# Kernel tuning notes

Measured on AMD Instinct MI355X. Metric: run time of the kernel, lower is better.

## Reference

```python
import jax, jax.numpy as jnp
import numpy as np

N = 4096
C = 64
B = 4
DIST_THRESHOLD = 0.5
ALPHA = 0.01
NEG_INF = -1e15


def setup_inputs() -> dict:
    key = jax.random.key(0)
    k1, k2, k3, k4, k5 = jax.random.split(key, 5)
    x = jax.random.normal(k1, (B, N, C), dtype=jnp.float32)
    dist_mat = jax.random.uniform(k2, (N, N), dtype=jnp.float32)
    proj_w = jax.random.normal(k3, (N, C, C), dtype=jnp.float32) / np.sqrt(C)
    proj_b = jax.random.normal(k4, (N, C), dtype=jnp.float32) * 0.01
    a_w = jax.random.normal(k5, (N, 2 * C), dtype=jnp.float32) / np.sqrt(2 * C)
    return {"x": x, "dist_mat": dist_mat, "proj_w": proj_w, "proj_b": proj_b, "a_w": a_w}


def reference(x, dist_mat, proj_w, proj_b, a_w):
    # Adjacency: (0 < dist < threshold), diagonal forced to 1.
    adj = (dist_mat > 0) & (dist_mat < DIST_THRESHOLD)
    adj = adj | jnp.eye(N, dtype=bool)

    # Per-node projection (GraphDense): h[b,n,:] = x[b,n,:] @ proj_w[n] + proj_b[n]
    h = jnp.einsum('bnc,nco->bno', x, proj_w) + proj_b  # [B, N, C]

    # Attention score: a[j] . concat(h_i, h_j) without materializing [B,N,N,2C].
    a_src, a_dst = a_w[:, :C], a_w[:, C:]               # each [N, C]
    s = jnp.einsum('bic,jc->bij', h, a_src) + jnp.einsum('bjc,jc->bj', h, a_dst)[:, None, :]
    s = jnp.where(s >= 0, s, ALPHA * s)                 # LeakyReLU
    s = jnp.where(adj[None, :, :], s, NEG_INF)          # mask non-edges
    att = jax.nn.softmax(s, axis=-1)                    # [B, N, N]

    # Weighted aggregation over neighbors.
    y = jnp.einsum('bij,bjc->bic', att, h)              # [B, N, C]
    return y
```

## Files before the change

### kernel.cpp

```cpp
#include <hip/hip_runtime.h>

#define N 4096
#define C 64
#define B 4
#define SHIFT 12.0f

typedef __attribute__((ext_vector_type(8))) short short8;
typedef __attribute__((ext_vector_type(4))) short s16x4;
typedef __attribute__((ext_vector_type(4))) float f32x4;
typedef unsigned long long u64;

#define MFMA16(a, b, c) __builtin_amdgcn_mfma_f32_16x16x32_bf16(a, b, c, 0, 0, 0)

__device__ __forceinline__ short f2bf(float f) {
    unsigned u = __builtin_bit_cast(unsigned, f);
    u += 0x7fffu + ((u >> 16) & 1u);
    return (short)(u >> 16);
}

__global__ __launch_bounds__(256) void mask_kernel(const float* __restrict__ dist,
                                                   u64* __restrict__ msk) {
    const int wave = threadIdx.x >> 6, lane = threadIdx.x & 63;
    const int i = blockIdx.x * 4 + wave;
    const float* row = dist + (size_t)i * N;
#pragma unroll 8
    for (int jb = 0; jb < N / 64; jb++) {
        float d = row[jb * 64 + lane];
        u64 m = __ballot(d > 0.f && d < 0.5f);
        int dj = i - jb * 64;
        if (dj >= 0 && dj < 64) m |= (1ull << dj);
        if (lane == 0) msk[(size_t)i * (N / 64) + jb] = m;
    }
}

__global__ __launch_bounds__(256) void proj_kernel(
    const float* __restrict__ x,
    const float* __restrict__ proj_w,
    const float* __restrict__ proj_b,
    const float* __restrict__ a_w,
    short* __restrict__ h_bf,
    short* __restrict__ a_srcb,
    float* __restrict__ e2)
{
    __shared__ float lds_w[4][64 * 64];
    __shared__ float lds_x[4][B][C];

    const int tid = threadIdx.x;
    const int wave = tid >> 6;
    const int lane = tid & 63;
    const int n = blockIdx.x * 4 + wave;
    const float* Wn = proj_w + (size_t)n * C * C;

    float4 wbuf[16];
#pragma unroll
    for (int it = 0; it < 16; it++)
        wbuf[it] = *(const float4*)(Wn + it * 256 + lane * 4);
#pragma unroll
    for (int b = 0; b < B; b++)
        lds_x[wave][b][lane] = x[((size_t)b * N + n) * C + lane];
#pragma unroll
    for (int it = 0; it < 16; it++)
        *(float4*)&lds_w[wave][it * 256 + lane * 4] = wbuf[it];

    const int o = lane;
    float acc[B];
    float pb = proj_b[(size_t)n * C + o];
#pragma unroll
    for (int b = 0; b < B; b++) acc[b] = pb;

#pragma unroll 4
    for (int c4 = 0; c4 < C; c4 += 4) {
        f32x4 xq[B];
#pragma unroll
        for (int b = 0; b < B; b++) xq[b] = *(const f32x4*)&lds_x[wave][b][c4];
#pragma unroll
        for (int k = 0; k < 4; k++) {
            float w = lds_w[wave][(c4 + k) * C + o];
#pragma unroll
            for (int b = 0; b < B; b++) acc[b] = fmaf(xq[b][k], w, acc[b]);
        }
    }

    float adst = a_w[(size_t)n * (2 * C) + C + o];
    a_srcb[(size_t)n * C + o] = f2bf(a_w[(size_t)n * (2 * C) + o]);
#pragma unroll
    for (int b = 0; b < B; b++) {
        h_bf[((size_t)b * N + n) * C + o] = f2bf(acc[b]);
        float prod = acc[b] * adst;
#pragma unroll
        for (int off = 32; off; off >>= 1) prod += __shfl_xor(prod, off, 64);
        if (lane == 0) e2[b * N + n] = prod - SHIFT;
    }
}

__global__ __launch_bounds__(256) void transpose_kernel(const short* __restrict__ h_bf,
                                                        short* __restrict__ hT_bf) {
    __shared__ short tile[64][72];
    const int t = threadIdx.x;
    const int b = blockIdx.y;
    const int n0 = blockIdx.x * 64;
    {
        int r = t >> 2, cs = (t & 3) * 16;
        const short* src = h_bf + ((size_t)b * N + n0 + r) * C + cs;
#pragma unroll
        for (int q = 0; q < 4; q++)
            *(s16x4*)&tile[r][cs + q * 4] = *(const s16x4*)(src + q * 4);
    }
    __syncthreads();
    {
        int c = t >> 2, ns = (t & 3) * 16;
        short v[16];
#pragma unroll
        for (int k = 0; k < 16; k++) v[k] = tile[ns + k][c];
        short* dst = hT_bf + (size_t)b * C * N + (size_t)c * N + n0 + ns;
        *(short8*)dst = *(short8*)&v[0];
        *(short8*)(dst + 8) = *(short8*)&v[8];
    }
}

__global__ __launch_bounds__(256) void attn_kernel(
    const u64* __restrict__ msk,
    const short* __restrict__ h_bf,
    const short* __restrict__ hT_bf,
    const short* __restrict__ a_srcb,
    const float* __restrict__ e2,
    float* __restrict__ part_y,
    float* __restrict__ part_l,
    int JS, int S, int mode)
{
    __shared__ float lds_e2[4][512];

    const int tid = threadIdx.x;
    const int wave = tid >> 6;
    const int lane = tid & 63;
    const int cl = lane & 15;
    const int rg = lane >> 4;
    const int rg8 = rg * 8;
    const int b = wave;
    const int sy = blockIdx.x % S;
    const int ix = blockIdx.x / S;
    const int i0 = ix * 32;
    const int jbeg = sy * JS;
    const bool e2lds = (JS <= 512);

    if (e2lds) {
        for (int q = lane * 4; q < JS; q += 256)
            *(f32x4*)&lds_e2[wave][q] = *(const f32x4*)(e2 + (size_t)b * N + jbeg + q);
    }

    short8 bfr[2][2];
#pragma unroll
    for (int u = 0; u < 2; u++) {
        const short* hrow = h_bf + ((size_t)b * N + i0 + u * 16 + cl) * C;
        bfr[u][0] = *(const short8*)(hrow + rg8);
        bfr[u][1] = *(const short8*)(hrow + 32 + rg8);
    }

    const u64* mr[2] = {msk + (size_t)(i0 + cl) * (N / 64),
                        msk + (size_t)(i0 + 16 + cl) * (N / 64)};

    f32x4 yacc[2][4];
#pragma unroll
    for (int u = 0; u < 2; u++)
#pragma unroll
        for (int t = 0; t < 4; t++) { f32x4 z = {0.f, 0.f, 0.f, 0.f}; yacc[u][t] = z; }
    float l_s[2] = {0.f, 0.f};

    const int jr = ((cl >> 2) << 3) | (cl & 3);
    const short* abase = a_srcb + (size_t)(jr) * C + rg8;

    short8 an0[4], an1[4];
#pragma unroll
    for (int t = 0; t < 4; t++) {
        const short* arow = abase + (size_t)(jbeg + (t >> 1) * 32 + (t & 1) * 4) * C;
        an0[t] = *(const short8*)(arow);
        an1[t] = *(const short8*)(arow + 32);
    }
    u64 mb0 = mr[0][jbeg >> 6], mb1 = mr[1][jbeg >> 6];

    for (int j0 = jbeg; j0 < jbeg + JS; j0 += 64) {
        const int jp = (j0 + 64 < jbeg + JS) ? j0 + 64 : jbeg;
        const u64 mb[2] = {mb0, mb1};

        short8 a0[4], a1[4];
#pragma unroll
        for (int t = 0; t < 4; t++) { a0[t] = an0[t]; a1[t] = an1[t]; }

        short8 h0[4], h1[4];
#pragma unroll
        for (int t = 0; t < 4; t++) {
            const short* hc = hT_bf + (size_t)b * C * N + (size_t)(t * 16 + cl) * N + j0 + rg8;
            h0[t] = *(const short8*)(hc);
            h1[t] = *(const short8*)(hc + 32);
        }
#pragma unroll
        for (int t = 0; t < 4; t++) {
            const short* arow = abase + (size_t)(jp + (t >> 1) * 32 + (t & 1) * 4) * C;
            an0[t] = *(const short8*)(arow);
            an1[t] = *(const short8*)(arow + 32);
        }
        u64 nb0 = mr[0][jp >> 6], nb1 = mr[1][jp >> 6];

        f32x4 st[2][4];
#pragma unroll
        for (int t = 0; t < 4; t++) {
            const int tq = t >> 1, tr = t & 1;
            const int off = tq * 32 + tr * 4 + rg8;
            f32x4 eq;
            if (e2lds) eq = *(const f32x4*)&lds_e2[wave][j0 - jbeg + off];
            else       eq = *(const f32x4*)(e2 + (size_t)b * N + j0 + off);
            const int sh = rg8 + tr * 4;
#pragma unroll
            for (int u = 0; u < 2; u++) {
                unsigned w32 = tq ? (unsigned)(mb[u] >> 32) : (unsigned)mb[u];
                unsigned ws = w32 >> sh;
                f32x4 z;
#pragma unroll
                for (int r = 0; r < 4; r++)
                    z[r] = ((ws >> r) & 1u) ? eq[r] : -1e30f;
                z = MFMA16(a0[t], bfr[u][0], z);
                z = MFMA16(a1[t], bfr[u][1], z);
                st[u][t] = z;
            }
        }

        short8 pa[2][2];
#pragma unroll
        for (int u = 0; u < 2; u++) {
            float ls = 0.f;
            short8 q0, q1;
#pragma unroll
            for (int t = 0; t < 4; t++) {
#pragma unroll
                for (int r = 0; r < 4; r++) {
                    float sv = st[u][t][r];
                    float pv = __expf(fmaxf(sv, fmaf(0.01f, sv, -11.88f)));
                    ls += pv;
                    short bv = f2bf(pv);
                    if (t < 2) q0[(t & 1) * 4 + r] = bv;
                    else       q1[(t & 1) * 4 + r] = bv;
                }
            }
            l_s[u] += ls;
            pa[u][0] = q0;
            pa[u][1] = q1;
        }

#pragma unroll
        for (int t = 0; t < 4; t++) {
            yacc[0][t] = MFMA16(pa[0][0], h0[t], yacc[0][t]);
            yacc[0][t] = MFMA16(pa[0][1], h1[t], yacc[0][t]);
            yacc[1][t] = MFMA16(pa[1][0], h0[t], yacc[1][t]);
            yacc[1][t] = MFMA16(pa[1][1], h1[t], yacc[1][t]);
        }
        mb0 = nb0; mb1 = nb1;
    }

#pragma unroll
    for (int u = 0; u < 2; u++) {
        l_s[u] += __shfl_xor(l_s[u], 16, 64);
        l_s[u] += __shfl_xor(l_s[u], 32, 64);
    }

    if (mode) {
#pragma unroll
        for (int u = 0; u < 2; u++) {
            int li = __builtin_bit_cast(int, l_s[u]);
            f32x4 l4;
#pragma unroll
            for (int r = 0; r < 4; r++)
                l4[r] = __builtin_bit_cast(float,
                        __builtin_amdgcn_ds_bpermute((rg * 4 + r) << 2, li));
#pragma unroll
            for (int t = 0; t < 4; t++)
#pragma unroll
                for (int r = 0; r < 4; r++)
                    part_y[((size_t)b * N + i0 + u * 16 + rg * 4 + r) * C + t * 16 + cl] =
                        yacc[u][t][r] / l4[r];
        }
    } else {
        size_t sb = (size_t)(sy * B + b) * N;
#pragma unroll
        for (int u = 0; u < 2; u++) {
#pragma unroll
            for (int t = 0; t < 4; t++)
#pragma unroll
                for (int r = 0; r < 4; r++)
                    part_y[(sb + i0 + u * 16 + rg * 4 + r) * C + t * 16 + cl] = yacc[u][t][r];
            if (lane < 16) part_l[sb + i0 + u * 16 + lane] = l_s[u];
        }
    }
}

__global__ __launch_bounds__(256) void combine_kernel(
    const float* __restrict__ part_y, const float* __restrict__ part_l,
    float* __restrict__ out, int S)
{
    int g = blockIdx.x * 256 + threadIdx.x;
    int c4 = (g & 15) * 4;
    int row = (g >> 4) & (N - 1);
    int b = g >> 16;
    int bn = b * N + row;
    f32x4 y = {0.f, 0.f, 0.f, 0.f};
    float l = 0.f;
    if (S == 8) {
#pragma unroll
        for (int s = 0; s < 8; s++) {
            l += part_l[s * (B * N) + bn];
            f32x4 v = *(const f32x4*)&part_y[((size_t)s * B * N + bn) * C + c4];
#pragma unroll
            for (int r = 0; r < 4; r++) y[r] += v[r];
        }
    } else {
        for (int s = 0; s < S; s++) {
            l += part_l[s * (B * N) + bn];
            f32x4 v = *(const f32x4*)&part_y[((size_t)s * B * N + bn) * C + c4];
#pragma unroll
            for (int r = 0; r < 4; r++) y[r] += v[r];
        }
    }
    float inv = 1.f / l;
    f32x4 o;
#pragma unroll
    for (int r = 0; r < 4; r++) o[r] = y[r] * inv;
    *(f32x4*)&out[(size_t)g * 4] = o;
}

extern "C" void kernel_launch(void* const* d_in, const int* in_sizes, int n_in,
                              void* d_out, int out_size, void* d_ws, size_t ws_size,
                              hipStream_t stream) {
    const float* x      = (const float*)d_in[0];
    const float* dist   = (const float*)d_in[1];
    const float* proj_w = (const float*)d_in[2];
    const float* proj_b = (const float*)d_in[3];
    const float* a_w    = (const float*)d_in[4];
    float* out = (float*)d_out;

    char* ws = (char*)d_ws;
    short* h_bf   = (short*)(ws);
    short* hT_bf  = (short*)(ws + (2u << 20));
    short* a_srcb = (short*)(ws + (4u << 20));
    float* e2     = (float*)(ws + (4u << 20) + (512u << 10));
    u64*   msk    = (u64*)  (ws + (5u << 20));
    float* part_l = (float*)(ws + (7u << 20));
    float* part_y = (float*)(ws + (8u << 20));

    proj_kernel<<<N / 4, 256, 0, stream>>>(x, proj_w, proj_b, a_w, h_bf, a_srcb, e2);
    transpose_kernel<<<dim3(N / 64, B), 256, 0, stream>>>(h_bf, hT_bf);
    mask_kernel<<<N / 4, 256, 0, stream>>>(dist, msk);

    int S = 8;
    while (S > 1 && (8u << 20) + (size_t)S * B * N * C * 4 > ws_size) S >>= 1;
    bool direct = ((8u << 20) + (size_t)B * N * C * 4 > ws_size);

    if (direct) {
        attn_kernel<<<N / 32, 256, 0, stream>>>(
            msk, h_bf, hT_bf, a_srcb, e2, out, part_l, N, 1, 1);
    } else {
        attn_kernel<<<(N / 32) * S, 256, 0, stream>>>(
            msk, h_bf, hT_bf, a_srcb, e2, part_y, part_l, N / S, S, 0);
        combine_kernel<<<(B * N * C / 4) / 256, 256, 0, stream>>>(part_y, part_l, out, S);
    }
}
```

Measured before the change: 274.5 us.

## Fuse mask build and h transpose into the projection kernel

Measured after the change: 296.3 us. 1.08x slower.

```diff
diff --git a/kernel.cpp b/kernel.cpp
--- a/kernel.cpp
+++ b/kernel.cpp
@@ -18,32 +18,21 @@
     return (short)(u >> 16);
 }
 
-__global__ __launch_bounds__(256) void mask_kernel(const float* __restrict__ dist,
-                                                   u64* __restrict__ msk) {
-    const int wave = threadIdx.x >> 6, lane = threadIdx.x & 63;
-    const int i = blockIdx.x * 4 + wave;
-    const float* row = dist + (size_t)i * N;
-#pragma unroll 8
-    for (int jb = 0; jb < N / 64; jb++) {
-        float d = row[jb * 64 + lane];
-        u64 m = __ballot(d > 0.f && d < 0.5f);
-        int dj = i - jb * 64;
-        if (dj >= 0 && dj < 64) m |= (1ull << dj);
-        if (lane == 0) msk[(size_t)i * (N / 64) + jb] = m;
-    }
-}
-
 __global__ __launch_bounds__(256) void proj_kernel(
     const float* __restrict__ x,
+    const float* __restrict__ dist,
     const float* __restrict__ proj_w,
     const float* __restrict__ proj_b,
     const float* __restrict__ a_w,
     short* __restrict__ h_bf,
+    short* __restrict__ hT_bf,
     short* __restrict__ a_srcb,
-    float* __restrict__ e2)
+    float* __restrict__ e2,
+    u64* __restrict__ msk)
 {
     __shared__ float lds_w[4][64 * 64];
     __shared__ float lds_x[4][B][C];
+    __shared__ short lds_h[B][4][C];
 
     const int tid = threadIdx.x;
     const int wave = tid >> 6;
@@ -58,6 +47,19 @@
 #pragma unroll
     for (int b = 0; b < B; b++)
         lds_x[wave][b][lane] = x[((size_t)b * N + n) * C + lane];
+
+    {
+        const float* drow = dist + (size_t)n * N;
+#pragma unroll 8
+        for (int jb = 0; jb < N / 64; jb++) {
+            float d = drow[jb * 64 + lane];
+            u64 m = __ballot(d > 0.f && d < 0.5f);
+            int dj = n - jb * 64;
+            if (dj >= 0 && dj < 64) m |= (1ull << dj);
+            if (lane == 0) msk[(size_t)n * (N / 64) + jb] = m;
+        }
+    }
+
 #pragma unroll
     for (int it = 0; it < 16; it++)
         *(float4*)&lds_w[wave][it * 256 + lane * 4] = wbuf[it];
@@ -85,36 +87,22 @@
     a_srcb[(size_t)n * C + o] = f2bf(a_w[(size_t)n * (2 * C) + o]);
 #pragma unroll
     for (int b = 0; b < B; b++) {
-        h_bf[((size_t)b * N + n) * C + o] = f2bf(acc[b]);
+        short hv = f2bf(acc[b]);
+        h_bf[((size_t)b * N + n) * C + o] = hv;
+        lds_h[b][wave][o] = hv;
         float prod = acc[b] * adst;
 #pragma unroll
         for (int off = 32; off; off >>= 1) prod += __shfl_xor(prod, off, 64);
         if (lane == 0) e2[b * N + n] = prod - SHIFT;
     }
-}
-
-__global__ __launch_bounds__(256) void transpose_kernel(const short* __restrict__ h_bf,
-                                                        short* __restrict__ hT_bf) {
-    __shared__ short tile[64][72];
-    const int t = threadIdx.x;
-    const int b = blockIdx.y;
-    const int n0 = blockIdx.x * 64;
-    {
-        int r = t >> 2, cs = (t & 3) * 16;
-        const short* src = h_bf + ((size_t)b * N + n0 + r) * C + cs;
-#pragma unroll
-        for (int q = 0; q < 4; q++)
-            *(s16x4*)&tile[r][cs + q * 4] = *(const s16x4*)(src + q * 4);
-    }
+
     __syncthreads();
     {
-        int c = t >> 2, ns = (t & 3) * 16;
-        short v[16];
-#pragma unroll
-        for (int k = 0; k < 16; k++) v[k] = tile[ns + k][c];
-        short* dst = hT_bf + (size_t)b * C * N + (size_t)c * N + n0 + ns;
-        *(short8*)dst = *(short8*)&v[0];
-        *(short8*)(dst + 8) = *(short8*)&v[8];
+        const int b = wave, c = lane;
+        s16x4 v;
+#pragma unroll
+        for (int k = 0; k < 4; k++) v[k] = lds_h[b][k][c];
+        *(s16x4*)&hT_bf[(size_t)b * C * N + (size_t)c * N + blockIdx.x * 4] = v;
     }
 }
 
@@ -345,9 +333,8 @@
     float* part_l = (float*)(ws + (7u << 20));
     float* part_y = (float*)(ws + (8u << 20));
 
-    proj_kernel<<<N / 4, 256, 0, stream>>>(x, proj_w, proj_b, a_w, h_bf, a_srcb, e2);
-    transpose_kernel<<<dim3(N / 64, B), 256, 0, stream>>>(h_bf, hT_bf);
-    mask_kernel<<<N / 4, 256, 0, stream>>>(dist, msk);
+    proj_kernel<<<N / 4, 256, 0, stream>>>(x, dist, proj_w, proj_b, a_w,
+                                           h_bf, hT_bf, a_srcb, e2, msk);
 
     int S = 8;
     while (S > 1 && (8u << 20) + (size_t)S * B * N * C * 4 > ws_size) S >>= 1;
```
